# Kernel tuning notes

Measured on AMD Instinct MI355X. Metric: run time of the kernel, lower is better.

## Reference

```python
import jax, jax.numpy as jnp
import numpy as np

EPS = 2.220446049250313e-16  # sys.float_info.epsilon, as in repo's feature_normalize
H_BW = 0.1  # bandwidth h (forward default)


def _feature_normalize(f):
    # L2 normalize over channel dim (dim=1) of [B, C, H, W]
    norm = jnp.sqrt(jnp.sum(f * f, axis=1, keepdims=True)) + EPS
    return f / norm


def setup_inputs() -> dict:
    key = jax.random.key(0)
    k1, k2 = jax.random.split(key)
    shape = (4, 256, 64, 64)
    return {
        "X_features": jax.random.normal(k1, shape, dtype=jnp.float32),
        "Y_features": jax.random.normal(k2, shape, dtype=jnp.float32),
    }


def reference(X_features, Y_features):
    B, C = X_features.shape[0], X_features.shape[1]
    # feature centering (opt.PONO = False branch): subtract Y's per-channel spatial mean
    y_mean = jnp.mean(Y_features.reshape(B, C, -1), axis=-1)[:, :, None, None]
    Xc = X_features - y_mean
    Yc = Y_features - y_mean
    # channel-wise L2 normalize, then flatten spatial dims -> [B, C, N]
    Xn = _feature_normalize(Xc).reshape(B, C, -1)
    Yn = _feature_normalize(Yc).reshape(B, C, -1)
    # pairwise cosine distance d: [B, N, N]
    d = 1.0 - jnp.einsum("bcn,bcm->bnm", Xn, Yn)
    # relative distance normalization by row-min
    d_min = jnp.min(d, axis=-1, keepdims=True)
    d_norm = d / (d_min + 0.001)
    # softmax-like contextual similarity weights
    w = jnp.exp((1.0 - d_norm) / H_BW)
    A_ij = w / jnp.sum(w, axis=-1, keepdims=True)
    # per-sample contextual similarity and loss
    CX = jnp.mean(jnp.max(A_ij, axis=-1), axis=1)  # [B]
    loss = -jnp.log(CX)
    return loss
```

## Files before the change

### kernel.cpp

```cpp
#include <hip/hip_runtime.h>
#include <hip/hip_bf16.h>
#include <stdint.h>


#define Bn 4
#define Cn 256
#define Nn 4096

typedef float  f32x16 __attribute__((ext_vector_type(16)));
typedef __bf16 bf16x8 __attribute__((ext_vector_type(8)));

#define GLD16(gp, lp) __builtin_amdgcn_global_load_lds(                      \
    (const __attribute__((address_space(1))) void*)(gp),                     \
    (__attribute__((address_space(3))) void*)(lp), 16, 0, 0)

#define LDbf(base, off) (*(const bf16x8*)((base) + (off)))

__global__ __launch_bounds__(256) void k_mean(const float* __restrict__ Y,
                                              float* __restrict__ ymean) {
  const int bc = blockIdx.x;
  const float4* p4 = (const float4*)(Y + (size_t)bc * 4096);
  float s = 0.f;
  #pragma unroll
  for (int i = 0; i < 4; ++i) {
    float4 v = p4[threadIdx.x + i * 256];
    s += (v.x + v.y) + (v.z + v.w);
  }
  #pragma unroll
  for (int m = 1; m < 64; m <<= 1) s += __shfl_xor(s, m);
  __shared__ float part[4];
  if ((threadIdx.x & 63) == 0) part[threadIdx.x >> 6] = s;
  __syncthreads();
  if (threadIdx.x == 0)
    ymean[bc] = (part[0] + part[1] + part[2] + part[3]) * (1.0f / 4096.0f);
}

__global__ __launch_bounds__(256) void k_pack(const float* __restrict__ X,
                                              const float* __restrict__ Y,
                                              const float* __restrict__ ymean,
                                              __hip_bfloat16* __restrict__ Xp,
                                              __hip_bfloat16* __restrict__ Yp,
                                              float* __restrict__ nx2,
                                              float* __restrict__ ny2) {
  const int n0 = blockIdx.x * 64, c0 = blockIdx.y * 64, b = blockIdx.z;
  __shared__ float tile[64][65];
  __shared__ float mu[64];
  const int t  = threadIdx.x;
  const int tc = t >> 6, tn = t & 63;
  const int oc = t & 63, on = t >> 6;
  if (t < 64) mu[t] = ymean[b * 256 + c0 + t];
  __syncthreads();
  #pragma unroll 4
  for (int i = 0; i < 16; ++i) {
    int cl = i * 4 + tc;
    tile[cl][tn] = X[((size_t)b * 256 + c0 + cl) * 4096 + n0 + tn] - mu[cl];
  }
  __syncthreads();
  #pragma unroll 2
  for (int i = 0; i < 16; ++i) {
    int nl = i * 4 + on;
    float v = tile[oc][nl];
    Xp[((size_t)b * 4096 + n0 + nl) * 256 + c0 + oc] = __float2bfloat16(v);
    float sq = v * v;
    #pragma unroll
    for (int m = 1; m < 64; m <<= 1) sq += __shfl_xor(sq, m);
    if (oc == 0) atomicAdd(nx2 + b * 4096 + n0 + nl, sq);
  }
  __syncthreads();
  #pragma unroll 4
  for (int i = 0; i < 16; ++i) {
    int cl = i * 4 + tc;
    tile[cl][tn] = Y[((size_t)b * 256 + c0 + cl) * 4096 + n0 + tn] - mu[cl];
  }
  __syncthreads();
  #pragma unroll 2
  for (int i = 0; i < 16; ++i) {
    int nl = i * 4 + on;
    float v = tile[oc][nl];
    Yp[((size_t)b * 4096 + n0 + nl) * 256 + c0 + oc] = __float2bfloat16(v);
    float sq = v * v;
    #pragma unroll
    for (int m = 1; m < 64; m <<= 1) sq += __shfl_xor(sq, m);
    if (oc == 0) atomicAdd(ny2 + b * 4096 + n0 + nl, sq);
  }
}

template<int PASS>
__global__ __launch_bounds__(512, 2) void k_pass(const __hip_bfloat16* __restrict__ Xp,
                                                 const __hip_bfloat16* __restrict__ Yp,
                                                 const float* __restrict__ nx2,
                                                 const float* __restrict__ ny2,
                                                 float* __restrict__ rmax_part,
                                                 float* __restrict__ ssum_part) {
  __shared__ __align__(16) char XsB[128 * 512];
  __shared__ __align__(16) char YsB2[2][256 * 128];
  __shared__ float invnyL[2048];
  __shared__ float redm[2][2][2][16][4];
  __shared__ float2 lammu[128];

  const int tid = threadIdx.x;
  const int lane = tid & 63;
  const int w = tid >> 6;
  const int rg = w >> 2, cs = w & 3;
  const int l31 = lane & 31, hi = lane >> 5;

  const int L = blockIdx.x;
  const int b = (L & 7) >> 1, half = L & 1;
  const int rowtile = L >> 3;
  const int rowg0 = b * Nn + rowtile * 128;
  const int colg0 = half * 2048;

  const char* Xg = (const char*)(Xp + (size_t)rowg0 * Cn);
  const char* Yg = (const char*)(Yp + ((size_t)b * Nn + colg0) * Cn);

  #pragma unroll
  for (int i = 0; i < 4; ++i) {
    int c = tid + i * 512;
    invnyL[c] = rsqrtf(ny2[b * Nn + colg0 + c]);
  }
  if constexpr (PASS == 2) {
    if (tid < 128) {
      int rowg = rowg0 + tid;
      float mg = fmaxf(rmax_part[rowg], rmax_part[Bn * Nn + rowg]);
      float invnx = rsqrtf(nx2[rowg]);
      float smax = mg * invnx;
      float lam = (10.0f / (1.001f - smax)) * invnx * 1.44269504f;
      lammu[tid] = make_float2(lam, lam * mg);
    }
  }
  __syncthreads();

  float lamr[2][16], mur[2][16];
  if constexpr (PASS == 2) {
    #pragma unroll
    for (int ai = 0; ai < 2; ++ai)
      #pragma unroll
      for (int r = 0; r < 16; ++r) {
        int rloc = rg * 64 + ai * 32 + (r & 3) + 8 * (r >> 2) + 4 * hi;
        float2 lm = lammu[rloc];
        lamr[ai][r] = lm.x; mur[ai][r] = lm.y;
      }
  }

  #pragma unroll
  for (int s = 0; s < 8; ++s) {
    int row = s * 16 + (tid >> 5);
    GLD16(Xg + row * 512 + (((tid & 31) * 16) ^ ((row & 15) << 4)),
          XsB + s * 8192 + tid * 16);
  }
  int yoff[4];
  #pragma unroll
  for (int i = 0; i < 4; ++i) {
    int m = i * 64 + (tid >> 3);
    yoff[i] = m * 512 + (((tid & 7) * 16) ^ ((m & 7) << 4));
  }
  auto stageY = [&](int q) {
    const char* src = Yg + (size_t)((q >> 2) * 131072 + (q & 3) * 128);
    char* dst = YsB2[q & 1];
    #pragma unroll
    for (int i = 0; i < 4; ++i)
      GLD16(src + yoff[i], dst + i * 8192 + tid * 16);
  };
  stageY(0);

  const int arow0 = rg * 64 + l31;
  const int aswz = (arow0 & 15) << 4;
  const int brow0 = cs * 64 + l31;
  const int bswz = (brow0 & 7) << 4;

  f32x16 acc[2][2];
  #pragma unroll
  for (int ai = 0; ai < 2; ++ai)
    #pragma unroll
    for (int bj = 0; bj < 2; ++bj) acc[ai][bj] = (f32x16)0.0f;
  float rmax[2][16], ssum[2][16];
  #pragma unroll
  for (int ai = 0; ai < 2; ++ai)
    #pragma unroll
    for (int r = 0; r < 16; ++r) { rmax[ai][r] = -3.0e38f; ssum[ai][r] = 0.f; }

  for (int p = 0; p < 32; ++p) {
    if (p < 31) { stageY(p + 1); asm volatile("s_waitcnt vmcnt(4)" ::: "memory"); }
    else        { asm volatile("s_waitcnt vmcnt(0)" ::: "memory"); }
    __builtin_amdgcn_s_barrier();

    const char* yb = YsB2[p & 1];
    const int kpB = (p & 3) << 7;
    __builtin_amdgcn_s_setprio(1);
    #pragma unroll
    for (int s = 0; s < 4; ++s) {
      const int kb = (s << 5) + (hi << 4);
      bf16x8 a0 = LDbf(XsB, arow0 * 512 + ((kpB + kb) ^ aswz));
      bf16x8 a1 = LDbf(XsB, (arow0 + 32) * 512 + ((kpB + kb) ^ aswz));
      bf16x8 b0 = LDbf(yb, brow0 * 128 + (kb ^ bswz));
      bf16x8 b1 = LDbf(yb, (brow0 + 32) * 128 + (kb ^ bswz));
      acc[0][0] = __builtin_amdgcn_mfma_f32_32x32x16_bf16(a0, b0, acc[0][0], 0, 0, 0);
      acc[0][1] = __builtin_amdgcn_mfma_f32_32x32x16_bf16(a0, b1, acc[0][1], 0, 0, 0);
      acc[1][0] = __builtin_amdgcn_mfma_f32_32x32x16_bf16(a1, b0, acc[1][0], 0, 0, 0);
      acc[1][1] = __builtin_amdgcn_mfma_f32_32x32x16_bf16(a1, b1, acc[1][1], 0, 0, 0);
    }
    __builtin_amdgcn_s_setprio(0);

    if ((p & 3) == 3) {
      const int cb = (p >> 2) * 256 + cs * 64 + l31;
      const float iny0 = invnyL[cb], iny1 = invnyL[cb + 32];
      #pragma unroll
      for (int ai = 0; ai < 2; ++ai)
        #pragma unroll
        for (int r = 0; r < 16; ++r) {
          if constexpr (PASS == 1) {
            rmax[ai][r] = fmaxf(rmax[ai][r],
                                fmaxf(acc[ai][0][r] * iny0, acc[ai][1][r] * iny1));
          } else {
            float e = exp2f(fmaf(lamr[ai][r], acc[ai][0][r] * iny0, -mur[ai][r]))
                    + exp2f(fmaf(lamr[ai][r], acc[ai][1][r] * iny1, -mur[ai][r]));
            ssum[ai][r] += e;
          }
          acc[ai][0][r] = 0.f; acc[ai][1][r] = 0.f;
        }
    }
    __builtin_amdgcn_s_barrier();
  }

  #pragma unroll
  for (int ai = 0; ai < 2; ++ai)
    #pragma unroll
    for (int r = 0; r < 16; ++r) {
      float v = (PASS == 1) ? rmax[ai][r] : ssum[ai][r];
      #pragma unroll
      for (int m = 1; m < 32; m <<= 1) {
        float o = __shfl_xor(v, m);
        v = (PASS == 1) ? fmaxf(v, o) : (v + o);
      }
      if (l31 == 0) redm[rg][hi][ai][r][cs] = v;
    }
  __syncthreads();
  if (tid < 128) {
    const int rgg = tid >> 6, rr = tid & 63;
    const int aii = (rr >> 5) & 1, r32 = rr & 31;
    const int hh = (r32 >> 2) & 1;
    const int reg = (r32 & 3) | (((r32 >> 3) & 3) << 2);
    float v0 = redm[rgg][hh][aii][reg][0], v1 = redm[rgg][hh][aii][reg][1];
    float v2 = redm[rgg][hh][aii][reg][2], v3 = redm[rgg][hh][aii][reg][3];
    if constexpr (PASS == 1)
      rmax_part[half * (Bn * Nn) + rowg0 + tid] = fmaxf(fmaxf(v0, v1), fmaxf(v2, v3));
    else
      ssum_part[half * (Bn * Nn) + rowg0 + tid] = v0 + v1 + v2 + v3;
  }
}

__global__ __launch_bounds__(256) void k_fin(const float* __restrict__ ssum_part,
                                             float* __restrict__ out) {
  const int b = blockIdx.x;
  float s = 0.f;
  #pragma unroll 4
  for (int i = 0; i < 16; ++i) {
    int row = b * Nn + threadIdx.x + i * 256;
    s += 1.0f / (ssum_part[row] + ssum_part[Bn * Nn + row]);
  }
  #pragma unroll
  for (int m = 1; m < 64; m <<= 1) s += __shfl_xor(s, m);
  __shared__ float part[4];
  if ((threadIdx.x & 63) == 0) part[threadIdx.x >> 6] = s;
  __syncthreads();
  if (threadIdx.x == 0)
    out[b] = -logf((part[0] + part[1] + part[2] + part[3]) * (1.0f / (float)Nn));
}

extern "C" void kernel_launch(void* const* d_in, const int* in_sizes, int n_in,
                              void* d_out, int out_size, void* d_ws, size_t ws_size,
                              hipStream_t stream) {
  const float* X = (const float*)d_in[0];
  const float* Y = (const float*)d_in[1];
  float* out = (float*)d_out;
  char* ws = (char*)d_ws;

  __hip_bfloat16* Xp = (__hip_bfloat16*)ws;
  __hip_bfloat16* Yp = (__hip_bfloat16*)(ws + 8388608);
  float* nx2  = (float*)(ws + 16777216);
  float* ny2  = nx2 + 16384;
  float* rmax = ny2 + 16384;
  float* ssum = rmax + 32768;
  float* ymean = ssum + 32768;

  hipMemsetAsync(nx2, 0, 2 * 16384 * sizeof(float), stream);
  k_mean  <<<Bn * Cn, 256, 0, stream>>>(Y, ymean);
  k_pack  <<<dim3(Nn / 64, Cn / 64, Bn), 256, 0, stream>>>(X, Y, ymean, Xp, Yp, nx2, ny2);
  k_pass<1><<<256, 512, 0, stream>>>(Xp, Yp, nx2, ny2, rmax, ssum);
  k_pass<2><<<256, 512, 0, stream>>>(Xp, Yp, nx2, ny2, rmax, ssum);
  k_fin   <<<Bn, 256, 0, stream>>>(ssum, out);
}
```

Before: 195.2 us.

## Hold X operands in registers, triple-buffer Y tiles, compute inverse norms in pack

```diff
diff --git a/kernel.cpp b/kernel.cpp
--- a/kernel.cpp
+++ b/kernel.cpp
@@ -15,6 +15,7 @@
     (__attribute__((address_space(3))) void*)(lp), 16, 0, 0)
 
 #define LDbf(base, off) (*(const bf16x8*)((base) + (off)))
+#define MFMA32(a, b, c) __builtin_amdgcn_mfma_f32_32x32x16_bf16((a), (b), (c), 0, 0, 0)
 
 __global__ __launch_bounds__(256) void k_mean(const float* __restrict__ Y,
                                               float* __restrict__ ymean) {
@@ -40,69 +41,77 @@
                                               const float* __restrict__ ymean,
                                               __hip_bfloat16* __restrict__ Xp,
                                               __hip_bfloat16* __restrict__ Yp,
-                                              float* __restrict__ nx2,
-                                              float* __restrict__ ny2) {
-  const int n0 = blockIdx.x * 64, c0 = blockIdx.y * 64, b = blockIdx.z;
+                                              float* __restrict__ invnx,
+                                              float* __restrict__ invny) {
+  const int n0 = blockIdx.x * 64, b = blockIdx.y;
+  __shared__ float mu[256];
   __shared__ float tile[64][65];
-  __shared__ float mu[64];
+  __shared__ float part[8][64];
   const int t  = threadIdx.x;
   const int tc = t >> 6, tn = t & 63;
   const int oc = t & 63, on = t >> 6;
-  if (t < 64) mu[t] = ymean[b * 256 + c0 + t];
-  __syncthreads();
-  #pragma unroll 4
-  for (int i = 0; i < 16; ++i) {
-    int cl = i * 4 + tc;
-    tile[cl][tn] = X[((size_t)b * 256 + c0 + cl) * 4096 + n0 + tn] - mu[cl];
-  }
-  __syncthreads();
-  #pragma unroll 2
-  for (int i = 0; i < 16; ++i) {
-    int nl = i * 4 + on;
-    float v = tile[oc][nl];
-    Xp[((size_t)b * 4096 + n0 + nl) * 256 + c0 + oc] = __float2bfloat16(v);
-    float sq = v * v;
-    #pragma unroll
-    for (int m = 1; m < 64; m <<= 1) sq += __shfl_xor(sq, m);
-    if (oc == 0) atomicAdd(nx2 + b * 4096 + n0 + nl, sq);
-  }
-  __syncthreads();
-  #pragma unroll 4
-  for (int i = 0; i < 16; ++i) {
-    int cl = i * 4 + tc;
-    tile[cl][tn] = Y[((size_t)b * 256 + c0 + cl) * 4096 + n0 + tn] - mu[cl];
-  }
-  __syncthreads();
-  #pragma unroll 2
-  for (int i = 0; i < 16; ++i) {
-    int nl = i * 4 + on;
-    float v = tile[oc][nl];
-    Yp[((size_t)b * 4096 + n0 + nl) * 256 + c0 + oc] = __float2bfloat16(v);
-    float sq = v * v;
-    #pragma unroll
-    for (int m = 1; m < 64; m <<= 1) sq += __shfl_xor(sq, m);
-    if (oc == 0) atomicAdd(ny2 + b * 4096 + n0 + nl, sq);
+  mu[t] = ymean[b * 256 + t];
+  __syncthreads();
+  float psx = 0.f, psy = 0.f;
+  for (int cc = 0; cc < 4; ++cc) {
+    #pragma unroll 4
+    for (int i = 0; i < 16; ++i) {
+      int cl = i * 4 + tc;
+      float v = X[((size_t)b * 256 + cc * 64 + cl) * 4096 + n0 + tn] - mu[cc * 64 + cl];
+      tile[cl][tn] = v;
+      psx += v * v;
+    }
+    __syncthreads();
+    #pragma unroll 4
+    for (int i = 0; i < 16; ++i) {
+      int nl = i * 4 + on;
+      Xp[((size_t)b * 4096 + n0 + nl) * 256 + cc * 64 + oc] = __float2bfloat16(tile[oc][nl]);
+    }
+    __syncthreads();
+    #pragma unroll 4
+    for (int i = 0; i < 16; ++i) {
+      int cl = i * 4 + tc;
+      float v = Y[((size_t)b * 256 + cc * 64 + cl) * 4096 + n0 + tn] - mu[cc * 64 + cl];
+      tile[cl][tn] = v;
+      psy += v * v;
+    }
+    __syncthreads();
+    #pragma unroll 4
+    for (int i = 0; i < 16; ++i) {
+      int nl = i * 4 + on;
+      Yp[((size_t)b * 4096 + n0 + nl) * 256 + cc * 64 + oc] = __float2bfloat16(tile[oc][nl]);
+    }
+    __syncthreads();
+  }
+  part[tc][tn] = psx;
+  part[4 + tc][tn] = psy;
+  __syncthreads();
+  if (t < 64)
+    invnx[b * 4096 + n0 + t] = rsqrtf(part[0][t] + part[1][t] + part[2][t] + part[3][t]);
+  else if (t < 128) {
+    int u = t - 64;
+    invny[b * 4096 + n0 + u] = rsqrtf(part[4][u] + part[5][u] + part[6][u] + part[7][u]);
   }
 }
 
 template<int PASS>
 __global__ __launch_bounds__(512, 2) void k_pass(const __hip_bfloat16* __restrict__ Xp,
                                                  const __hip_bfloat16* __restrict__ Yp,
-                                                 const float* __restrict__ nx2,
-                                                 const float* __restrict__ ny2,
+                                                 const float* __restrict__ invnx,
+                                                 const float* __restrict__ invny,
                                                  float* __restrict__ rmax_part,
                                                  float* __restrict__ ssum_part) {
-  __shared__ __align__(16) char XsB[128 * 512];
-  __shared__ __align__(16) char YsB2[2][256 * 128];
+  __shared__ __align__(16) char YsL[3][32768];
   __shared__ float invnyL[2048];
   __shared__ float redm[2][2][2][16][4];
-  __shared__ float2 lammu[128];
+  __shared__ float2 lammuL[128];
 
   const int tid = threadIdx.x;
   const int lane = tid & 63;
   const int w = tid >> 6;
   const int rg = w >> 2, cs = w & 3;
   const int l31 = lane & 31, hi = lane >> 5;
+  const int hi16 = hi << 4;
 
   const int L = blockIdx.x;
   const int b = (L & 7) >> 1, half = L & 1;
@@ -110,123 +119,141 @@
   const int rowg0 = b * Nn + rowtile * 128;
   const int colg0 = half * 2048;
 
-  const char* Xg = (const char*)(Xp + (size_t)rowg0 * Cn);
-  const char* Yg = (const char*)(Yp + ((size_t)b * Nn + colg0) * Cn);
-
-  #pragma unroll
-  for (int i = 0; i < 4; ++i) {
-    int c = tid + i * 512;
-    invnyL[c] = rsqrtf(ny2[b * Nn + colg0 + c]);
-  }
+  const char* Xgb = (const char*)Xp + (size_t)rowg0 * 512;
+  const char* Yg  = (const char*)(Yp + ((size_t)b * Nn + colg0) * Cn);
+
+  bf16x8 A[4][4][2];
+  #pragma unroll
+  for (int kp = 0; kp < 4; ++kp)
+    #pragma unroll
+    for (int s = 0; s < 4; ++s)
+      #pragma unroll
+      for (int ai = 0; ai < 2; ++ai)
+        A[kp][s][ai] = *(const bf16x8*)(Xgb + (size_t)(rg * 64 + ai * 32 + l31) * 512
+                                            + ((kp * 4 + s) * 32 + hi16));
+
+  ((float4*)invnyL)[tid] = ((const float4*)(invny + b * Nn + colg0))[tid];
   if constexpr (PASS == 2) {
     if (tid < 128) {
       int rowg = rowg0 + tid;
       float mg = fmaxf(rmax_part[rowg], rmax_part[Bn * Nn + rowg]);
-      float invnx = rsqrtf(nx2[rowg]);
-      float smax = mg * invnx;
-      float lam = (10.0f / (1.001f - smax)) * invnx * 1.44269504f;
-      lammu[tid] = make_float2(lam, lam * mg);
-    }
-  }
-  __syncthreads();
-
-  float lamr[2][16], mur[2][16];
-  if constexpr (PASS == 2) {
-    #pragma unroll
-    for (int ai = 0; ai < 2; ++ai)
-      #pragma unroll
-      for (int r = 0; r < 16; ++r) {
-        int rloc = rg * 64 + ai * 32 + (r & 3) + 8 * (r >> 2) + 4 * hi;
-        float2 lm = lammu[rloc];
-        lamr[ai][r] = lm.x; mur[ai][r] = lm.y;
-      }
-  }
-
-  #pragma unroll
-  for (int s = 0; s < 8; ++s) {
-    int row = s * 16 + (tid >> 5);
-    GLD16(Xg + row * 512 + (((tid & 31) * 16) ^ ((row & 15) << 4)),
-          XsB + s * 8192 + tid * 16);
-  }
+      float ix = invnx[rowg];
+      float smax = mg * ix;
+      float lam = (10.0f / (1.001f - smax)) * ix * 1.44269504f;
+      lammuL[tid] = make_float2(lam, lam * mg);
+    }
+  }
+  __syncthreads();
+
   int yoff[4];
   #pragma unroll
   for (int i = 0; i < 4; ++i) {
     int m = i * 64 + (tid >> 3);
     yoff[i] = m * 512 + (((tid & 7) * 16) ^ ((m & 7) << 4));
   }
-  auto stageY = [&](int q) {
-    const char* src = Yg + (size_t)((q >> 2) * 131072 + (q & 3) * 128);
-    char* dst = YsB2[q & 1];
-    #pragma unroll
-    for (int i = 0; i < 4; ++i)
-      GLD16(src + yoff[i], dst + i * 8192 + tid * 16);
-  };
-  stageY(0);
-
-  const int arow0 = rg * 64 + l31;
-  const int aswz = (arow0 & 15) << 4;
+
+#define STAGE_HALF(q, h)                                                      \
+  { const int q_ = (q);                                                       \
+    const char* src_ = Yg + (size_t)((q_ >> 2) * 131072 + (q_ & 3) * 128);    \
+    char* dst_ = YsL[q_ % 3];                                                 \
+    GLD16(src_ + yoff[2 * (h)],     dst_ + (2 * (h)) * 8192 + tid * 16);      \
+    GLD16(src_ + yoff[2 * (h) + 1], dst_ + (2 * (h) + 1) * 8192 + tid * 16); }
+
+  STAGE_HALF(0, 0); STAGE_HALF(0, 1);
+  STAGE_HALF(1, 0); STAGE_HALF(1, 1);
+
   const int brow0 = cs * 64 + l31;
-  const int bswz = (brow0 & 7) << 4;
+  const int bswz  = (brow0 & 7) << 4;
 
   f32x16 acc[2][2];
   #pragma unroll
   for (int ai = 0; ai < 2; ++ai)
     #pragma unroll
     for (int bj = 0; bj < 2; ++bj) acc[ai][bj] = (f32x16)0.0f;
-  float rmax[2][16], ssum[2][16];
+  float accR[2][16];
   #pragma unroll
   for (int ai = 0; ai < 2; ++ai)
     #pragma unroll
-    for (int r = 0; r < 16; ++r) { rmax[ai][r] = -3.0e38f; ssum[ai][r] = 0.f; }
-
-  for (int p = 0; p < 32; ++p) {
-    if (p < 31) { stageY(p + 1); asm volatile("s_waitcnt vmcnt(4)" ::: "memory"); }
-    else        { asm volatile("s_waitcnt vmcnt(0)" ::: "memory"); }
-    __builtin_amdgcn_s_barrier();
-
-    const char* yb = YsB2[p & 1];
-    const int kpB = (p & 3) << 7;
-    __builtin_amdgcn_s_setprio(1);
-    #pragma unroll
-    for (int s = 0; s < 4; ++s) {
-      const int kb = (s << 5) + (hi << 4);
-      bf16x8 a0 = LDbf(XsB, arow0 * 512 + ((kpB + kb) ^ aswz));
-      bf16x8 a1 = LDbf(XsB, (arow0 + 32) * 512 + ((kpB + kb) ^ aswz));
-      bf16x8 b0 = LDbf(yb, brow0 * 128 + (kb ^ bswz));
-      bf16x8 b1 = LDbf(yb, (brow0 + 32) * 128 + (kb ^ bswz));
-      acc[0][0] = __builtin_amdgcn_mfma_f32_32x32x16_bf16(a0, b0, acc[0][0], 0, 0, 0);
-      acc[0][1] = __builtin_amdgcn_mfma_f32_32x32x16_bf16(a0, b1, acc[0][1], 0, 0, 0);
-      acc[1][0] = __builtin_amdgcn_mfma_f32_32x32x16_bf16(a1, b0, acc[1][0], 0, 0, 0);
-      acc[1][1] = __builtin_amdgcn_mfma_f32_32x32x16_bf16(a1, b1, acc[1][1], 0, 0, 0);
-    }
-    __builtin_amdgcn_s_setprio(0);
-
-    if ((p & 3) == 3) {
-      const int cb = (p >> 2) * 256 + cs * 64 + l31;
-      const float iny0 = invnyL[cb], iny1 = invnyL[cb + 32];
-      #pragma unroll
-      for (int ai = 0; ai < 2; ++ai)
-        #pragma unroll
-        for (int r = 0; r < 16; ++r) {
-          if constexpr (PASS == 1) {
-            rmax[ai][r] = fmaxf(rmax[ai][r],
-                                fmaxf(acc[ai][0][r] * iny0, acc[ai][1][r] * iny1));
-          } else {
-            float e = exp2f(fmaf(lamr[ai][r], acc[ai][0][r] * iny0, -mur[ai][r]))
-                    + exp2f(fmaf(lamr[ai][r], acc[ai][1][r] * iny1, -mur[ai][r]));
-            ssum[ai][r] += e;
-          }
-          acc[ai][0][r] = 0.f; acc[ai][1][r] = 0.f;
-        }
-    }
-    __builtin_amdgcn_s_barrier();
-  }
+    for (int r = 0; r < 16; ++r) accR[ai][r] = (PASS == 1) ? -3.0e38f : 0.f;
+
+#define HARVEST()                                                             \
+  { const int cb = mt * 256 + cs * 64 + l31;                                  \
+    const float iny0 = invnyL[cb], iny1 = invnyL[cb + 32];                    \
+    _Pragma("unroll")                                                         \
+    for (int ai = 0; ai < 2; ++ai) {                                          \
+      _Pragma("unroll")                                                       \
+      for (int r = 0; r < 16; ++r) {                                          \
+        if constexpr (PASS == 1) {                                            \
+          accR[ai][r] = fmaxf(accR[ai][r],                                    \
+              fmaxf(acc[ai][0][r] * iny0, acc[ai][1][r] * iny1));             \
+        } else {                                                              \
+          float2 lm = lammuL[rg * 64 + ai * 32 + (r & 3) + 8 * (r >> 2) + 4 * hi]; \
+          accR[ai][r] += exp2f(fmaf(lm.x, acc[ai][0][r] * iny0, -lm.y))       \
+                       + exp2f(fmaf(lm.x, acc[ai][1][r] * iny1, -lm.y));      \
+        }                                                                     \
+        acc[ai][0][r] = 0.f; acc[ai][1][r] = 0.f;                             \
+      } } }
+
+#define TILE(KP, WAITS, DO_STAGE)                                             \
+  { const int p_ = mt * 4 + (KP);                                             \
+    if (DO_STAGE) STAGE_HALF(p_ + 2, 0);                                      \
+    asm volatile("s_waitcnt vmcnt(" WAITS ")" ::: "memory");                  \
+    asm volatile("s_barrier" ::: "memory");                                   \
+    const char* yb_ = YsL[p_ % 3];                                            \
+    bf16x8 b00 = LDbf(yb_, brow0 * 128 + ((0 + hi16) ^ bswz));                \
+    bf16x8 b01 = LDbf(yb_, (brow0 + 32) * 128 + ((0 + hi16) ^ bswz));         \
+    bf16x8 b10 = LDbf(yb_, brow0 * 128 + ((32 + hi16) ^ bswz));               \
+    bf16x8 b11 = LDbf(yb_, (brow0 + 32) * 128 + ((32 + hi16) ^ bswz));        \
+    if (DO_STAGE) STAGE_HALF(p_ + 2, 1);                                      \
+    __builtin_amdgcn_s_setprio(1);                                            \
+    acc[0][0] = MFMA32(A[KP][0][0], b00, acc[0][0]);                          \
+    acc[0][1] = MFMA32(A[KP][0][0], b01, acc[0][1]);                          \
+    acc[1][0] = MFMA32(A[KP][0][1], b00, acc[1][0]);                          \
+    acc[1][1] = MFMA32(A[KP][0][1], b01, acc[1][1]);                          \
+    acc[0][0] = MFMA32(A[KP][1][0], b10, acc[0][0]);                          \
+    acc[0][1] = MFMA32(A[KP][1][0], b11, acc[0][1]);                          \
+    acc[1][0] = MFMA32(A[KP][1][1], b10, acc[1][0]);                          \
+    acc[1][1] = MFMA32(A[KP][1][1], b11, acc[1][1]);                          \
+    __builtin_amdgcn_s_setprio(0);                                            \
+    bf16x8 b20 = LDbf(yb_, brow0 * 128 + ((64 + hi16) ^ bswz));               \
+    bf16x8 b21 = LDbf(yb_, (brow0 + 32) * 128 + ((64 + hi16) ^ bswz));        \
+    bf16x8 b30 = LDbf(yb_, brow0 * 128 + ((96 + hi16) ^ bswz));               \
+    bf16x8 b31 = LDbf(yb_, (brow0 + 32) * 128 + ((96 + hi16) ^ bswz));        \
+    __builtin_amdgcn_s_setprio(1);                                            \
+    acc[0][0] = MFMA32(A[KP][2][0], b20, acc[0][0]);                          \
+    acc[0][1] = MFMA32(A[KP][2][0], b21, acc[0][1]);                          \
+    acc[1][0] = MFMA32(A[KP][2][1], b20, acc[1][0]);                          \
+    acc[1][1] = MFMA32(A[KP][2][1], b21, acc[1][1]);                          \
+    acc[0][0] = MFMA32(A[KP][3][0], b30, acc[0][0]);                          \
+    acc[0][1] = MFMA32(A[KP][3][0], b31, acc[0][1]);                          \
+    acc[1][0] = MFMA32(A[KP][3][1], b30, acc[1][0]);                          \
+    acc[1][1] = MFMA32(A[KP][3][1], b31, acc[1][1]);                          \
+    __builtin_amdgcn_s_setprio(0);                                            \
+    if ((KP) == 3) HARVEST();                                                 \
+    asm volatile("s_barrier" ::: "memory"); }
+
+  for (int mt = 0; mt < 7; ++mt) {
+    TILE(0, "6", true)
+    TILE(1, "6", true)
+    TILE(2, "6", true)
+    TILE(3, "6", true)
+  }
+  {
+    const int mt = 7;
+    TILE(0, "6", true)
+    TILE(1, "6", true)
+    TILE(2, "4", false)
+    TILE(3, "0", false)
+  }
+#undef TILE
+#undef HARVEST
+#undef STAGE_HALF
 
   #pragma unroll
   for (int ai = 0; ai < 2; ++ai)
     #pragma unroll
     for (int r = 0; r < 16; ++r) {
-      float v = (PASS == 1) ? rmax[ai][r] : ssum[ai][r];
+      float v = accR[ai][r];
       #pragma unroll
       for (int m = 1; m < 32; m <<= 1) {
         float o = __shfl_xor(v, m);
@@ -277,16 +304,15 @@
 
   __hip_bfloat16* Xp = (__hip_bfloat16*)ws;
   __hip_bfloat16* Yp = (__hip_bfloat16*)(ws + 8388608);
-  float* nx2  = (float*)(ws + 16777216);
-  float* ny2  = nx2 + 16384;
-  float* rmax = ny2 + 16384;
-  float* ssum = rmax + 32768;
+  float* invnx = (float*)(ws + 16777216);
+  float* invny = invnx + 16384;
+  float* rmax  = invny + 16384;
+  float* ssum  = rmax + 32768;
   float* ymean = ssum + 32768;
 
-  hipMemsetAsync(nx2, 0, 2 * 16384 * sizeof(float), stream);
   k_mean  <<<Bn * Cn, 256, 0, stream>>>(Y, ymean);
-  k_pack  <<<dim3(Nn / 64, Cn / 64, Bn), 256, 0, stream>>>(X, Y, ymean, Xp, Yp, nx2, ny2);
-  k_pass<1><<<256, 512, 0, stream>>>(Xp, Yp, nx2, ny2, rmax, ssum);
-  k_pass<2><<<256, 512, 0, stream>>>(Xp, Yp, nx2, ny2, rmax, ssum);
+  k_pack  <<<dim3(Nn / 64, Bn), 256, 0, stream>>>(X, Y, ymean, Xp, Yp, invnx, invny);
+  k_pass<1><<<256, 512, 0, stream>>>(Xp, Yp, invnx, invny, rmax, ssum);
+  k_pass<2><<<256, 512, 0, stream>>>(Xp, Yp, invnx, invny, rmax, ssum);
   k_fin   <<<Bn, 256, 0, stream>>>(ssum, out);
 }
```

Result: slower. 233.2 us (+19.4%).
